# Kernel optimization log

Measured on AMD Instinct MI355X. Metric: run time of the kernel, lower is better.

Reference implementation:

```python
import jax, jax.numpy as jnp
import numpy as np

SEQ, B, V, E, H, L = 64, 64, 32000, 512, 512, 2


def setup_inputs() -> dict:
    key = jax.random.key(0)
    ks = jax.random.split(key, 12)
    k = float(np.sqrt(1.0 / H))
    u = lambda kk, shape, a, b: jax.random.uniform(kk, shape, jnp.float32, a, b)
    return {
        "inputs": jax.random.randint(ks[0], (SEQ, B), 0, V),          # [T, B] token ids
        "hidden": jnp.zeros((L, B, H), jnp.float32),                   # initial hidden
        "emb": u(ks[1], (V, E), -0.1, 0.1),                            # embedding table
        "Wr_w": u(ks[2], (L, H, E + H), -k, k),                        # reset gate [L,H,2H]
        "Wr_b": u(ks[3], (L, H), -k, k),
        "Wz_w": u(ks[4], (L, H, E + H), -k, k),                        # update gate
        "Wz_b": u(ks[5], (L, H), -k, k),
        "Wh_w": u(ks[6], (L, H, E + H), -k, k),                        # candidate
        "Wh_b": u(ks[7], (L, H), -k, k),
        "out_w": u(ks[8], (V, H), -0.1, 0.1),                          # output projection
        "out_b": jnp.zeros((V,), jnp.float32),
    }


def reference(inputs, hidden, emb, Wr_w, Wr_b, Wz_w, Wz_b, Wh_w, Wh_b, out_w, out_b):
    # GRU recurrence over time via lax.scan (dropout disabled: dp_keep_prob=1.0)
    def step(h, tok):
        x = emb[tok]  # [B, E]
        new_h = []
        for i in range(L):  # fixed small layer loop
            hi = h[i]  # [B, H]
            cat = jnp.concatenate([x, hi], axis=1)  # [B, E+H]
            r = jax.nn.sigmoid(cat @ Wr_w[i].T + Wr_b[i])
            z = jax.nn.sigmoid(cat @ Wz_w[i].T + Wz_b[i])
            h_hat = jnp.tanh(jnp.concatenate([x, r * hi], axis=1) @ Wh_w[i].T + Wh_b[i])
            x = (1.0 - z) * hi + z * h_hat  # next layer input / new hidden
            new_h.append(x)
        logits_t = x @ out_w.T + out_b  # [B, V]
        return jnp.stack(new_h), logits_t

    hidden_final, logits = jax.lax.scan(step, hidden, inputs)
    return logits, hidden_final  # [T,B,V], [L,B,H]
```

## Files before the change

kernel.cpp:

```cpp
#include <hip/hip_runtime.h>

constexpr int NT = 64;
constexpr int NB = 64;
constexpr int NV = 32000;
constexpr int NE = 512;
constexpr int NH = 512;
constexpr int NPAIR = 16 * 250;

constexpr size_t SZ_OW  = (size_t)NV * NE;
constexpr size_t SZ_XE  = (size_t)NT * NB * NE;
constexpr size_t SZ_H   = (size_t)NB * NH;
constexpr size_t LOGITS = (size_t)NT * NB * NV;

typedef float f32x4 __attribute__((ext_vector_type(4)));
typedef int   i32x4 __attribute__((ext_vector_type(4)));
typedef short bf16x8 __attribute__((ext_vector_type(8)));
typedef short s16x4 __attribute__((ext_vector_type(4)));
typedef _Float16 f16x8 __attribute__((ext_vector_type(8)));

__device__ __forceinline__ unsigned short f2bf(float x) {
  unsigned u = __float_as_uint(x);
  u += 0x7FFFu + ((u >> 16) & 1u);
  return (unsigned short)(u >> 16);
}
__device__ __forceinline__ float bf2f(unsigned short s) {
  return __uint_as_float(((unsigned)s) << 16);
}
__device__ __forceinline__ void split2(float v, short* hi, short* lo) {
  unsigned short h = f2bf(v);
  *hi = (short)h;
  *lo = (short)f2bf(v - bf2f(h));
}
__device__ __forceinline__ f32x4 mma_bf16(bf16x8 a, bf16x8 b, f32x4 c) {
  return __builtin_amdgcn_mfma_f32_16x16x32_bf16(a, b, c, 0, 0, 0);
}
__device__ __forceinline__ f32x4 mma_f16(f16x8 a, f16x8 b, f32x4 c) {
  return __builtin_amdgcn_mfma_f32_16x16x32_f16(a, b, c, 0, 0, 0);
}
__device__ __forceinline__ float fast_sigmoid(float x) {
  return __builtin_amdgcn_rcpf(1.0f + __expf(-x));
}
__device__ __forceinline__ float fast_tanh(float x) {
  return 1.0f - 2.0f * __builtin_amdgcn_rcpf(1.0f + __expf(2.0f * x));
}

__device__ __forceinline__ void st_sc32u(unsigned* p, unsigned v) {
  asm volatile("global_store_dword %0, %1, off sc0 sc1" :: "v"(p), "v"(v) : "memory");
}
__device__ __forceinline__ void st_sc128(void* p, i32x4 v) {
  asm volatile("global_store_dwordx4 %0, %1, off sc0 sc1" :: "v"(p), "v"(v) : "memory");
}
__device__ __forceinline__ void st_nt(float* p, float v) {
  asm volatile("global_store_dword %0, %1, off nt" :: "v"(p), "v"(v) : "memory");
}
__device__ __forceinline__ unsigned ld_sc32u(const unsigned* p) {
  unsigned v;
  asm volatile("global_load_dword %0, %1, off sc0 sc1\n\ts_waitcnt vmcnt(0)"
               : "=v"(v) : "v"(p) : "memory");
  return v;
}

__device__ __forceinline__ void wait1(const unsigned* flags, int slot, unsigned thr) {
  while (ld_sc32u(&flags[(size_t)slot * 32]) < thr) {}
}
__device__ __forceinline__ void wave_poll4(const unsigned* flags, int slotBase, int cgBase,
                                           int rh, unsigned thr, int lane) {
  const unsigned* fp = &flags[(size_t)(slotBase + (cgBase + (lane & 3)) * 2 + rh) * 32];
  while (!__all((int)(ld_sc32u(fp) >= thr))) {}
}
__device__ __forceinline__ void wave_poll8(const unsigned* flags, int slotBase, int cgBase,
                                           int rh, unsigned thr, int lane) {
  const unsigned* fp = &flags[(size_t)(slotBase + (cgBase + (lane & 7)) * 2 + rh) * 32];
  while (!__all((int)(ld_sc32u(fp) >= thr))) {}
}

__device__ __forceinline__ void publish(unsigned* flags, int slot, unsigned val) {
  asm volatile("s_waitcnt vmcnt(0)" ::: "memory");
  __syncthreads();
  if (threadIdx.x == 0) st_sc32u(&flags[(size_t)slot * 32], val);
}

__global__ void k_prep(
    const float* __restrict__ outw, const int* __restrict__ toks,
    const float* __restrict__ emb, const float* __restrict__ hid,
    _Float16* OWf, short* XeHi, short* XeLo,
    short* X1Hi, short* X1Lo, short* h0Hi, short* h0Lo) {
  const size_t stride = (size_t)gridDim.x * blockDim.x;
  const size_t N1 = SZ_OW, N2 = N1 + SZ_XE, N3 = N2 + SZ_H, N4 = N3 + SZ_H;
  for (size_t x = (size_t)blockIdx.x * blockDim.x + threadIdx.x; x < N4; x += stride) {
    if (x < N1) {
      OWf[x] = (_Float16)outw[x];
    } else if (x < N2) {
      size_t p = x - N1;
      size_t r = p >> 9, c = p & 511u;
      int tok = toks[r];
      float v = emb[(size_t)tok * 512 + c];
      short hi, lo; split2(v, &hi, &lo);
      XeHi[p] = hi; XeLo[p] = lo;
    } else if (x < N3) {
      size_t p = x - N2;
      short hi, lo; split2(hid[p], &hi, &lo);
      h0Hi[p] = hi; h0Lo[p] = lo;
    } else {
      size_t p = x - N3;
      short hi, lo; split2(hid[SZ_H + p], &hi, &lo);
      X1Hi[p] = hi; X1Lo[p] = lo;
    }
  }
}

__device__ __forceinline__ void mmaP32(
    const short* __restrict__ aH, const short* __restrict__ aL, int base,
    const short* lsHi_, const short* lsLo_,
    f32x4 (&accH)[2], f32x4 (&accL)[2], int wave, int l15, int lq) {
  const int kq = wave >> 1, rhalf = wave & 1;
  const int r0 = rhalf * 16 + l15;
#pragma unroll
  for (int i = 0; i < 4; ++i) {
    const int ko = kq * 128 + i * 32 + lq * 8;
    const int kg = base + ko;
    const int e0 = (l15 * 1024 + kg) ^ ((l15 & 7) << 3);
    const int e1 = ((16 + l15) * 1024 + kg) ^ ((l15 & 7) << 3);
    bf16x8 bh0 = *(const bf16x8*)&lsHi_[e0];
    bf16x8 bl0 = *(const bf16x8*)&lsLo_[e0];
    bf16x8 bh1 = *(const bf16x8*)&lsHi_[e1];
    bf16x8 bl1 = *(const bf16x8*)&lsLo_[e1];
    bf16x8 ah = *(const bf16x8*)&aH[r0 * 512 + ko];
    bf16x8 al = *(const bf16x8*)&aL[r0 * 512 + ko];
    accH[0] = mma_bf16(ah, bh0, accH[0]);
    accH[1] = mma_bf16(ah, bh1, accH[1]);
    accL[0] = mma_bf16(al, bh0, accL[0]);
    accL[1] = mma_bf16(al, bh1, accL[1]);
    accL[0] = mma_bf16(ah, bl0, accL[0]);
    accL[1] = mma_bf16(ah, bl1, accL[1]);
  }
}
__device__ __forceinline__ void reduce4(float* lsRed_, f32x4 (&accH)[2], f32x4 (&accL)[2],
                                        f32x4 (&acc)[2], int wave, int l15, int lq) {
  const int kq = wave >> 1, rhalf = wave & 1;
  acc[0] = accH[0] + accL[0];
  acc[1] = accH[1] + accL[1];
  const int pos = l15 * 16 + lq * 4;
  if (kq) {
    *(f32x4*)&lsRed_[(((kq - 1) * 2 + rhalf) * 2 + 0) * 256 + pos] = acc[0];
    *(f32x4*)&lsRed_[(((kq - 1) * 2 + rhalf) * 2 + 1) * 256 + pos] = acc[1];
  }
  __syncthreads();
  if (!kq) {
#pragma unroll
    for (int s = 0; s < 3; ++s) {
      acc[0] += *(const f32x4*)&lsRed_[((s * 2 + rhalf) * 2 + 0) * 256 + pos];
      acc[1] += *(const f32x4*)&lsRed_[((s * 2 + rhalf) * 2 + 1) * 256 + pos];
    }
  }
  __syncthreads();
}

__device__ __forceinline__ void mmaD(
    const short* __restrict__ pAH, const short* __restrict__ pAL,
    int kloc0, int kkGlob0, const short* lsHi_, const short* lsLo_,
    f32x4 (&accH)[2], f32x4 (&accL)[2], int l15, int lq, int rhalf, int rowbase) {
  const int r0 = rowbase + rhalf * 16 + l15;
#pragma unroll 4
  for (int i = 0; i < 8; ++i) {
    const int kk = kkGlob0 + i * 32 + lq * 8;
    const int ka = kloc0 + i * 32 + lq * 8;
    const int e0 = (l15 * 1024 + kk) ^ ((l15 & 7) << 3);
    const int e1 = ((16 + l15) * 1024 + kk) ^ ((l15 & 7) << 3);
    bf16x8 bh0 = *(const bf16x8*)&lsHi_[e0];
    bf16x8 bl0 = *(const bf16x8*)&lsLo_[e0];
    bf16x8 bh1 = *(const bf16x8*)&lsHi_[e1];
    bf16x8 bl1 = *(const bf16x8*)&lsLo_[e1];
    bf16x8 ah = *(const bf16x8*)&pAH[r0 * 512 + ka];
    bf16x8 al = *(const bf16x8*)&pAL[r0 * 512 + ka];
    accH[0] = mma_bf16(ah, bh0, accH[0]);
    accH[1] = mma_bf16(ah, bh1, accH[1]);
    accL[0] = mma_bf16(al, bh0, accL[0]);
    accL[1] = mma_bf16(al, bh1, accL[1]);
    accL[0] = mma_bf16(ah, bl0, accL[0]);
    accL[1] = mma_bf16(ah, bl1, accL[1]);
  }
}
__device__ __forceinline__ void reduceD(float* lsRed_, f32x4 (&accH)[2], f32x4 (&accL)[2],
                                        f32x4 (&acc)[2], int wave, int l15, int lq) {
  acc[0] = accH[0] + accL[0];
  acc[1] = accH[1] + accL[1];
  const int pos = l15 * 16 + lq * 4;
  if (wave >= 2) {
    *(f32x4*)&lsRed_[((wave - 2) * 2 + 0) * 256 + pos] = acc[0];
    *(f32x4*)&lsRed_[((wave - 2) * 2 + 1) * 256 + pos] = acc[1];
  }
  __syncthreads();
  if (wave < 2) {
#pragma unroll
    for (int s = 0; s < 3; ++s) {
      const int slot = (wave & 1) + 2 * s;
      acc[0] += *(const f32x4*)&lsRed_[(slot * 2 + 0) * 256 + pos];
      acc[1] += *(const f32x4*)&lsRed_[(slot * 2 + 1) * 256 + pos];
    }
  }
  __syncthreads();
}

__device__ __forceinline__ void stage_weights(
    short* lsHi, short* lsLo, const float* srcBase0, const float* srcBase1,
    int jc, int tid) {
  for (int i = tid; i < 8192; i += 512) {
    const int j = i >> 8;
    const int k4 = (i & 255) << 2;
    const int g = jc + j;
    const float* src = (srcBase1 && g >= 512)
        ? (srcBase1 + (size_t)(g - 512) * 1024 + k4)
        : (srcBase0 + (size_t)g * 1024 + k4);
    f32x4 v = *(const f32x4*)src;
    s16x4 h4, l4;
#pragma unroll
    for (int q = 0; q < 4; ++q) { short hi, lo; split2(v[q], &hi, &lo); h4[q] = hi; l4[q] = lo; }
    const int els = (j * 1024 + k4) ^ ((j & 7) << 3);
    *(s16x4*)&lsHi[els] = h4;
    *(s16x4*)&lsLo[els] = l4;
  }
}

__device__ void gemm_loop(char* pool, int tid,
                          const _Float16* Af, const _Float16* Bw,
                          const float* bias, float* C,
                          unsigned* flags, unsigned* tcnt) {
  _Float16* lsA0 = (_Float16*)pool;
  _Float16* lsA1 = lsA0 + 128 * 64;
  _Float16* lsB  = lsA1 + 128 * 64;
  volatile int* bc = (volatile int*)(pool + 49152);
  const int wave = tid >> 6, lane = tid & 63, l15 = lane & 15, lq = lane >> 4;
  const int wr = (wave >> 2) * 64, wc = (wave & 3) * 32;
  unsigned lastR = 0;
  __syncthreads();
  for (;;) {
    if (tid == 0)
      *bc = (int)__hip_atomic_fetch_add(tcnt, 1u, __ATOMIC_RELAXED,
                                        __HIP_MEMORY_SCOPE_AGENT);
    __syncthreads();
    const int pr = *bc;
    __syncthreads();
    if (pr >= NPAIR) break;
    const int p = pr / 250, bn = pr - p * 250;
    const unsigned Rneed = 4u * (unsigned)p + 4u;
    if (lastR < Rneed) {
      if (tid < 32) {
        const unsigned* fp = &flags[(size_t)(160 + tid) * 32];
        while (ld_sc32u(fp) < Rneed) __builtin_amdgcn_s_sleep(8);
      }
      lastR = Rneed;
    }
    __syncthreads();
    f32x4 acc0[4][2] = {}, acc1[4][2] = {};
    const size_t arow0 = (size_t)p * 256;
    const size_t brow0 = (size_t)bn * 128;
    for (int kb = 0; kb < 512; kb += 64) {
#pragma unroll
      for (int i = 0; i < 2; ++i) {
        int c = tid + i * 512;
        int row = c >> 3, kc = (c & 7) * 8;
        int el = (row * 64 + kc) ^ ((row & 7) << 3);
        *(f16x8*)&lsA0[el] = *(const f16x8*)(Af + (arow0 + row) * 512 + kb + kc);
        *(f16x8*)&lsA1[el] = *(const f16x8*)(Af + (arow0 + 128 + row) * 512 + kb + kc);
        *(f16x8*)&lsB[el]  = *(const f16x8*)(Bw + (brow0 + row) * 512 + kb + kc);
      }
      __syncthreads();
#pragma unroll
      for (int k0 = 0; k0 < 64; k0 += 32) {
        const int kk = k0 + lq * 8;
        f16x8 af0[4], af1[4], bfr[2];
#pragma unroll
        for (int i = 0; i < 4; ++i) {
          int ra = wr + i * 16 + l15;
          int el = (ra * 64 + kk) ^ ((ra & 7) << 3);
          af0[i] = *(const f16x8*)&lsA0[el];
          af1[i] = *(const f16x8*)&lsA1[el];
        }
#pragma unroll
        for (int jt = 0; jt < 2; ++jt) {
          int rb = wc + jt * 16 + l15;
          bfr[jt] = *(const f16x8*)&lsB[(rb * 64 + kk) ^ ((rb & 7) << 3)];
        }
#pragma unroll
        for (int i = 0; i < 4; ++i)
#pragma unroll
          for (int jt = 0; jt < 2; ++jt) {
            acc0[i][jt] = mma_f16(af0[i], bfr[jt], acc0[i][jt]);
            acc1[i][jt] = mma_f16(af1[i], bfr[jt], acc1[i][jt]);
          }
      }
      __syncthreads();
    }
    const float b0v = bias[brow0 + wc + l15];
    const float b1v = bias[brow0 + wc + 16 + l15];
#pragma unroll
    for (int i = 0; i < 4; ++i) {
#pragma unroll
      for (int r = 0; r < 4; ++r) {
        const size_t row = arow0 + wr + i * 16 + lq * 4 + r;
        float* pa = C + row * (size_t)NV + brow0 + wc + l15;
        st_nt(pa, acc0[i][0][r] + b0v);
        st_nt(pa + 16, acc0[i][1][r] + b1v);
        float* pb = pa + (size_t)128 * NV;
        st_nt(pb, acc1[i][0][r] + b0v);
        st_nt(pb + 16, acc1[i][1][r] + b1v);
      }
    }
  }
}

__launch_bounds__(512, 1)
__global__ void k_main(
    const float* __restrict__ Wr, const float* __restrict__ Wz, const float* __restrict__ Wh,
    const float* __restrict__ Wrb, const float* __restrict__ Wzb, const float* __restrict__ Whb,
    const short* __restrict__ XeHi, const short* __restrict__ XeLo,
    short* X1Hi, short* X1Lo, _Float16* X1f16,
    short* h0Hi, short* h0Lo,
    short* rh0Hi, short* rh0Lo, short* rh1Hi, short* rh1Lo,
    float* z0, float* z1, float* hidOut,
    const _Float16* OWf, const float* outb, float* out,
    unsigned* flags, unsigned* tcnt) {
  __shared__ __align__(16) char pool[153600];
  short* lsHi = (short*)pool;
  short* lsLo = lsHi + 32 * 1024;
  float* lsRed = (float*)(pool + 131072);
  short* sH    = (short*)(pool + 131072);
  short* sL    = sH + 1024;
  float* sZA   = (float*)(pool + 131072);
  short* stH   = (short*)(pool + 143360);
  short* stL   = stH + 1024;
  float* sZ    = (float*)(pool + 147456);
  _Float16* sX = (_Float16*)(pool + 151552);

  const int wg = blockIdx.x;
  const int tid = threadIdx.x;
  const int wave = tid >> 6, lane = tid & 63, l15 = lane & 15, lq = lane >> 4;

  if (wg < 64) {
    const int cg = wg >> 1, rh = wg & 1, jc = cg * 32, rowbase = rh * 32;
    const bool isR = (jc < 512);
    stage_weights(lsHi, lsLo, Wr, Wz, jc, tid);
    float biasL0, biasL1;
    {
      const int j0 = jc + l15, j1 = j0 + 16;
      biasL0 = (j0 < 512) ? Wrb[j0] : Wzb[j0 - 512];
      biasL1 = (j1 < 512) ? Wrb[j1] : Wzb[j1 - 512];
    }
    __syncthreads();
    for (int t = 0; t < NT; ++t) {
      f32x4 accH[2] = {}, accL[2] = {};
      mmaP32(XeHi + (size_t)t * SZ_H + rowbase * 512,
             XeLo + (size_t)t * SZ_H + rowbase * 512, 0,
             lsHi, lsLo, accH, accL, wave, l15, lq);
      const short* hH = h0Hi + (size_t)t * SZ_H + rowbase * 512;
      const short* hL = h0Lo + (size_t)t * SZ_H + rowbase * 512;
      i32x4 pre;
      const int pbuf = tid >> 7, pq = tid & 127, prow = pq >> 2, pc = pq & 3;
      if (isR && tid < 256) {
        wait1(flags, 128 + ((jc >> 5) * 2 + rh), (unsigned)t);
        pre = *(const i32x4*)((pbuf ? hL : hH) + prow * 512 + jc + pc * 8);
      }
      wave_poll4(flags, 128, 4 * (wave >> 1), rh, (unsigned)t, lane);
      mmaP32(hH, hL, 512, lsHi, lsLo, accH, accL, wave, l15, lq);
      if (isR && tid < 256)
        *(i32x4*)&(pbuf ? stL : stH)[prow * 32 + pc * 8] = pre;
      f32x4 acc[2];
      reduce4(lsRed, accH, accL, acc, wave, l15, lq);
      if (wave < 2) {
#pragma unroll
        for (int ct = 0; ct < 2; ++ct) {
          const int jj = ct * 16 + l15;
          const float bv = ct ? biasL1 : biasL0;
#pragma unroll
          for (int r = 0; r < 4; ++r) {
            const int lb = wave * 16 + lq * 4 + r;
            const float s = fast_sigmoid(acc[ct][r] + bv);
            if (isR) {
              const float hv = bf2f((unsigned short)stH[lb * 32 + jj]) +
                               bf2f((unsigned short)stL[lb * 32 + jj]);
              short hi, lo; split2(s * hv, &hi, &lo);
              sH[lb * 32 + jj] = hi; sL[lb * 32 + jj] = lo;
            } else {
              sZA[lb * 32 + jj] = s;
            }
          }
        }
      }
      __syncthreads();
      if (isR) {
        if (tid < 256) {
          i32x4 v = *(const i32x4*)&(pbuf ? sL : sH)[prow * 32 + pc * 8];
          st_sc128((pbuf ? rh0Lo : rh0Hi) + (size_t)t * SZ_H +
                   (size_t)(rowbase + prow) * 512 + jc + pc * 8, v);
        }
      } else {
        if (tid < 256) {
          const int row = tid >> 3, c = tid & 7;
          i32x4 v = *(const i32x4*)&sZA[row * 32 + c * 4];
          st_sc128(z0 + (size_t)t * SZ_H + (size_t)(rowbase + row) * 512 +
                   (jc - 512) + c * 4, v);
        }
      }
      publish(flags, wg, (unsigned)(t + 1));
    }
  } else if (wg < 128) {
    const int idx = wg - 64, cg = idx >> 1, rh = idx & 1, jc = cg * 32, rowbase = rh * 32;
    const bool isR = (jc < 512);
    stage_weights(lsHi, lsLo, Wr + (size_t)512 * 1024, Wz + (size_t)512 * 1024, jc, tid);
    float biasL0, biasL1;
    {
      const int j0 = jc + l15, j1 = j0 + 16;
      biasL0 = (j0 < 512) ? Wrb[512 + j0] : Wzb[512 + j0 - 512];
      biasL1 = (j1 < 512) ? Wrb[512 + j1] : Wzb[512 + j1 - 512];
    }
    __syncthreads();
    for (int t = 0; t < NT; ++t) {
      const short* xH = h0Hi + (size_t)(t + 1) * SZ_H;
      const short* xL = h0Lo + (size_t)(t + 1) * SZ_H;
      const short* hH = X1Hi + (size_t)t * SZ_H;
      const short* hL = X1Lo + (size_t)t * SZ_H;
      i32x4 pre;
      const int pbuf = tid >> 7, pq = tid & 127, prow = pq >> 2, pc = pq & 3;
      if (isR && tid < 256) {
        wait1(flags, 160 + ((jc >> 5) * 2 + rh), (unsigned)t);
        pre = *(const i32x4*)((pbuf ? hL : hH) +
                              (size_t)(rowbase + prow) * 512 + jc + pc * 8);
      }
      f32x4 accH[2] = {}, accL[2] = {};
      {
        const int khalf = wave >> 1, rhalf = wave & 1;
        if (khalf < 2) wave_poll8(flags, 128, (khalf & 1) * 8, rh, (unsigned)(t + 1), lane);
        else           wave_poll8(flags, 160, (khalf & 1) * 8, rh, (unsigned)t, lane);
        const short* pAH = (khalf < 2) ? xH : hH;
        const short* pAL = (khalf < 2) ? xL : hL;
        mmaD(pAH, pAL, (khalf & 1) * 256, khalf * 256, lsHi, lsLo,
             accH, accL, l15, lq, rhalf, rowbase);
      }
      if (isR && tid < 256)
        *(i32x4*)&(pbuf ? stL : stH)[prow * 32 + pc * 8] = pre;
      f32x4 acc[2];
      reduceD(lsRed, accH, accL, acc, wave, l15, lq);
      if (wave < 2) {
#pragma unroll
        for (int ct = 0; ct < 2; ++ct) {
          const int jj = ct * 16 + l15;
          const float bv = ct ? biasL1 : biasL0;
#pragma unroll
          for (int r = 0; r < 4; ++r) {
            const int lb = wave * 16 + lq * 4 + r;
            const float s = fast_sigmoid(acc[ct][r] + bv);
            if (isR) {
              const float hv = bf2f((unsigned short)stH[lb * 32 + jj]) +
                               bf2f((unsigned short)stL[lb * 32 + jj]);
              short hi, lo; split2(s * hv, &hi, &lo);
              sH[lb * 32 + jj] = hi; sL[lb * 32 + jj] = lo;
            } else {
              sZA[lb * 32 + jj] = s;
            }
          }
        }
      }
      __syncthreads();
      if (isR) {
        if (tid < 256) {
          i32x4 v = *(const i32x4*)&(pbuf ? sL : sH)[prow * 32 + pc * 8];
          st_sc128((pbuf ? rh1Lo : rh1Hi) + (size_t)t * SZ_H +
                   (size_t)(rowbase + prow) * 512 + jc + pc * 8, v);
        }
      } else {
        if (tid < 256) {
          const int row = tid >> 3, c = tid & 7;
          i32x4 v = *(const i32x4*)&sZA[row * 32 + c * 4];
          st_sc128(z1 + (size_t)t * SZ_H + (size_t)(rowbase + row) * 512 +
                   (jc - 512) + c * 4, v);
        }
      }
      publish(flags, wg, (unsigned)(t + 1));
    }
  } else if (wg < 192) {
    const bool isL1 = (wg >= 160);
    const int idx = isL1 ? (wg - 160) : (wg - 128);
    const int cg = idx >> 1, rh = idx & 1, jc = cg * 32, rowbase = rh * 32;
    const int layer = isL1 ? 1 : 0;
    stage_weights(lsHi, lsLo, Wh + (size_t)layer * 512 * 1024, nullptr, jc, tid);
    const float biasL0 = Whb[layer * 512 + jc + l15];
    const float biasL1 = Whb[layer * 512 + jc + 16 + l15];
    __syncthreads();
    short* myHi = isL1 ? X1Hi : h0Hi;
    short* myLo = isL1 ? X1Lo : h0Lo;
    const short* rhHi_ = isL1 ? rh1Hi : rh0Hi;
    const short* rhLo_ = isL1 ? rh1Lo : rh0Lo;
    const float* zArr = isL1 ? z1 : z0;
    const int fbase = isL1 ? 64 : 0;
    for (int t = 0; t < NT; ++t) {
      const int pbuf = tid >> 7, pq = tid & 127, prow = pq >> 2, pc = pq & 3;
      if (tid < 256) {
        const short* src = (pbuf ? myLo : myHi) + (size_t)t * SZ_H +
                           (size_t)(rowbase + prow) * 512 + jc + pc * 8;
        *(i32x4*)&(pbuf ? stL : stH)[prow * 32 + pc * 8] = *(const i32x4*)src;
      }
      f32x4 accH[2] = {}, accL[2] = {};
      if (isL1) {
        wave_poll4(flags, 128, 4 * (wave >> 1), rh, (unsigned)(t + 1), lane);
        mmaP32(h0Hi + (size_t)(t + 1) * SZ_H + rowbase * 512,
               h0Lo + (size_t)(t + 1) * SZ_H + rowbase * 512, 0,
               lsHi, lsLo, accH, accL, wave, l15, lq);
      } else {
        mmaP32(XeHi + (size_t)t * SZ_H + rowbase * 512,
               XeLo + (size_t)t * SZ_H + rowbase * 512, 0,
               lsHi, lsLo, accH, accL, wave, l15, lq);
      }
      f32x4 zv;
      const int zrow = tid >> 3, zc = tid & 7;
      if (tid < 256) {
        wait1(flags, fbase + ((16 + (jc >> 5)) * 2 + rh), (unsigned)(t + 1));
        zv = *(const f32x4*)(zArr + (size_t)t * SZ_H +
                             (size_t)(rowbase + zrow) * 512 + jc + zc * 4);
      }
      wave_poll4(flags, fbase, 4 * (wave >> 1), rh, (unsigned)(t + 1), lane);
      mmaP32(rhHi_ + (size_t)t * SZ_H + rowbase * 512,
             rhLo_ + (size_t)t * SZ_H + rowbase * 512, 512,
             lsHi, lsLo, accH, accL, wave, l15, lq);
      if (tid < 256)
        *(f32x4*)&sZ[zrow * 32 + zc * 4] = zv;
      f32x4 acc[2];
      reduce4(lsRed, accH, accL, acc, wave, l15, lq);
      if (wave < 2) {
#pragma unroll
        for (int ct = 0; ct < 2; ++ct) {
          const int jj = ct * 16 + l15, j = jc + jj;
          const float bv = ct ? biasL1 : biasL0;
#pragma unroll
          for (int r = 0; r < 4; ++r) {
            const int lb = wave * 16 + lq * 4 + r;
            const float hh = fast_tanh(acc[ct][r] + bv);
            const float z = sZ[lb * 32 + jj];
            const float ho = bf2f((unsigned short)stH[lb * 32 + jj]) +
                             bf2f((unsigned short)stL[lb * 32 + jj]);
            const float hn = (1.0f - z) * ho + z * hh;
            short hi, lo; split2(hn, &hi, &lo);
            sH[lb * 32 + jj] = hi; sL[lb * 32 + jj] = lo;
            if (isL1) sX[lb * 32 + jj] = (_Float16)hn;
            if (t == NT - 1)
              hidOut[(size_t)layer * SZ_H + (size_t)(rowbase + lb) * 512 + j] = hn;
          }
        }
      }
      __syncthreads();
      if (tid < 256) {
        i32x4 v = *(const i32x4*)&(pbuf ? sL : sH)[prow * 32 + pc * 8];
        st_sc128((pbuf ? myLo : myHi) + (size_t)(t + 1) * SZ_H +
                 (size_t)(rowbase + prow) * 512 + jc + pc * 8, v);
      } else if (isL1 && tid < 384) {
        const int q = tid - 256, row = q >> 2, c = q & 3;
        i32x4 v = *(const i32x4*)&sX[row * 32 + c * 8];
        st_sc128(X1f16 + (size_t)t * SZ_H + (size_t)(rowbase + row) * 512 + jc + c * 8, v);
      }
      publish(flags, wg, (unsigned)(t + 1));
    }
  }
  gemm_loop(pool, tid, X1f16, OWf, outb, out, flags, tcnt);
}

extern "C" void kernel_launch(void* const* d_in, const int* in_sizes, int n_in,
                              void* d_out, int out_size, void* d_ws, size_t ws_size,
                              hipStream_t stream) {
  (void)in_sizes; (void)n_in; (void)out_size; (void)ws_size;
  const int*   toks = (const int*)d_in[0];
  const float* hid  = (const float*)d_in[1];
  const float* emb  = (const float*)d_in[2];
  const float* Wr   = (const float*)d_in[3];
  const float* Wrb  = (const float*)d_in[4];
  const float* Wz   = (const float*)d_in[5];
  const float* Wzb  = (const float*)d_in[6];
  const float* Wh   = (const float*)d_in[7];
  const float* Whb  = (const float*)d_in[8];
  const float* outw = (const float*)d_in[9];
  const float* outb = (const float*)d_in[10];
  float* out = (float*)d_out;

  char* base = (char*)d_ws;
  size_t off = 0;
  auto carve = [&](size_t bytes) -> char* {
    char* r = base + off;
    off = (off + bytes + 255) & ~(size_t)255;
    return r;
  };
  _Float16* OWf   = (_Float16*)carve(SZ_OW * 2);
  short*    XeHi  = (short*)carve(SZ_XE * 2);
  short*    XeLo  = (short*)carve(SZ_XE * 2);
  short*    X1Hi  = (short*)carve((size_t)(NT + 1) * SZ_H * 2);
  short*    X1Lo  = (short*)carve((size_t)(NT + 1) * SZ_H * 2);
  _Float16* X1f16 = (_Float16*)carve((size_t)NT * SZ_H * 2);
  short*    h0Hi  = (short*)carve((size_t)(NT + 1) * SZ_H * 2);
  short*    h0Lo  = (short*)carve((size_t)(NT + 1) * SZ_H * 2);
  short*    rh0Hi = (short*)carve((size_t)NT * SZ_H * 2);
  short*    rh0Lo = (short*)carve((size_t)NT * SZ_H * 2);
  short*    rh1Hi = (short*)carve((size_t)NT * SZ_H * 2);
  short*    rh1Lo = (short*)carve((size_t)NT * SZ_H * 2);
  float*    z0    = (float*)carve((size_t)NT * SZ_H * 4);
  float*    z1    = (float*)carve((size_t)NT * SZ_H * 4);
  unsigned* flags = (unsigned*)carve(32768);
  unsigned* tcnt  = (unsigned*)carve(256);

  hipMemsetAsync(flags, 0, 32768, stream);
  hipMemsetAsync(tcnt, 0, 256, stream);

  k_prep<<<2048, 256, 0, stream>>>(outw, toks, emb, hid,
                                   OWf, XeHi, XeLo, X1Hi, X1Lo, h0Hi, h0Lo);

  k_main<<<256, 512, 0, stream>>>(
      Wr, Wz, Wh, Wrb, Wzb, Whb, XeHi, XeLo,
      X1Hi, X1Lo, X1f16, h0Hi, h0Lo,
      rh0Hi, rh0Lo, rh1Hi, rh1Lo, z0, z1,
      out + LOGITS, OWf, outb, out, flags, tcnt);
}
```

Baseline: 698.4 us.

## Widen output GEMM tiles to 256x256 and merge flag polls into one wave poll

The output-projection GEMM tile grows from 256x128 to 256x256, giving 2000 work quads instead of 4000 pairs. Each A tile loaded into LDS now feeds twice as many MFMAs, and per-tile scheduling and flag-wait overhead is halved. The cost is a doubling of accumulator registers and a larger LDS footprint, which may cause spills. Separately, the single-thread wait1 spin and the wave-wide poll in the recurrent stages are folded into one wave poll, with one lane assigned to the extra flag, to cut serialized polling latency.

Result: no change. 703.2 us (+0.7%).

```diff
diff --git a/kernel.cpp b/kernel.cpp
--- a/kernel.cpp
+++ b/kernel.cpp
@@ -5,7 +5,7 @@
 constexpr int NV = 32000;
 constexpr int NE = 512;
 constexpr int NH = 512;
-constexpr int NPAIR = 16 * 250;
+constexpr int NQUAD = 16 * 125;
 
 constexpr size_t SZ_OW  = (size_t)NV * NE;
 constexpr size_t SZ_XE  = (size_t)NT * NB * NE;
@@ -60,18 +60,13 @@
   return v;
 }
 
-__device__ __forceinline__ void wait1(const unsigned* flags, int slot, unsigned thr) {
-  while (ld_sc32u(&flags[(size_t)slot * 32]) < thr) {}
+__device__ __forceinline__ void wave_poll(const unsigned* fp, unsigned thr) {
+  while (!__all((int)(ld_sc32u(fp) >= thr))) {}
 }
 __device__ __forceinline__ void wave_poll4(const unsigned* flags, int slotBase, int cgBase,
                                            int rh, unsigned thr, int lane) {
   const unsigned* fp = &flags[(size_t)(slotBase + (cgBase + (lane & 3)) * 2 + rh) * 32];
-  while (!__all((int)(ld_sc32u(fp) >= thr))) {}
-}
-__device__ __forceinline__ void wave_poll8(const unsigned* flags, int slotBase, int cgBase,
-                                           int rh, unsigned thr, int lane) {
-  const unsigned* fp = &flags[(size_t)(slotBase + (cgBase + (lane & 7)) * 2 + rh) * 32];
-  while (!__all((int)(ld_sc32u(fp) >= thr))) {}
+  wave_poll(fp, thr);
 }
 
 __device__ __forceinline__ void publish(unsigned* flags, int slot, unsigned val) {
@@ -227,9 +222,10 @@
                           const float* bias, float* C,
                           unsigned* flags, unsigned* tcnt) {
   _Float16* lsA0 = (_Float16*)pool;
-  _Float16* lsA1 = lsA0 + 128 * 64;
-  _Float16* lsB  = lsA1 + 128 * 64;
-  volatile int* bc = (volatile int*)(pool + 49152);
+  _Float16* lsA1 = lsA0 + 8192;
+  _Float16* lsB0 = lsA1 + 8192;
+  _Float16* lsB1 = lsB0 + 8192;
+  volatile int* bc = (volatile int*)(pool + 65536);
   const int wave = tid >> 6, lane = tid & 63, l15 = lane & 15, lq = lane >> 4;
   const int wr = (wave >> 2) * 64, wc = (wave & 3) * 32;
   unsigned lastR = 0;
@@ -241,8 +237,8 @@
     __syncthreads();
     const int pr = *bc;
     __syncthreads();
-    if (pr >= NPAIR) break;
-    const int p = pr / 250, bn = pr - p * 250;
+    if (pr >= NQUAD) break;
+    const int p = pr / 125, bq = pr - p * 125;
     const unsigned Rneed = 4u * (unsigned)p + 4u;
     if (lastR < Rneed) {
       if (tid < 32) {
@@ -252,9 +248,9 @@
       lastR = Rneed;
     }
     __syncthreads();
-    f32x4 acc0[4][2] = {}, acc1[4][2] = {};
+    f32x4 a00[4][2] = {}, a01[4][2] = {}, a10[4][2] = {}, a11[4][2] = {};
     const size_t arow0 = (size_t)p * 256;
-    const size_t brow0 = (size_t)bn * 128;
+    const size_t brow0 = (size_t)bq * 256;
     for (int kb = 0; kb < 512; kb += 64) {
 #pragma unroll
       for (int i = 0; i < 2; ++i) {
@@ -263,13 +259,14 @@
         int el = (row * 64 + kc) ^ ((row & 7) << 3);
         *(f16x8*)&lsA0[el] = *(const f16x8*)(Af + (arow0 + row) * 512 + kb + kc);
         *(f16x8*)&lsA1[el] = *(const f16x8*)(Af + (arow0 + 128 + row) * 512 + kb + kc);
-        *(f16x8*)&lsB[el]  = *(const f16x8*)(Bw + (brow0 + row) * 512 + kb + kc);
+        *(f16x8*)&lsB0[el] = *(const f16x8*)(Bw + (brow0 + row) * 512 + kb + kc);
+        *(f16x8*)&lsB1[el] = *(const f16x8*)(Bw + (brow0 + 128 + row) * 512 + kb + kc);
       }
       __syncthreads();
 #pragma unroll
       for (int k0 = 0; k0 < 64; k0 += 32) {
         const int kk = k0 + lq * 8;
-        f16x8 af0[4], af1[4], bfr[2];
+        f16x8 af0[4], af1[4], b0[2], b1[2];
 #pragma unroll
         for (int i = 0; i < 4; ++i) {
           int ra = wr + i * 16 + l15;
@@ -280,31 +277,41 @@
 #pragma unroll
         for (int jt = 0; jt < 2; ++jt) {
           int rb = wc + jt * 16 + l15;
-          bfr[jt] = *(const f16x8*)&lsB[(rb * 64 + kk) ^ ((rb & 7) << 3)];
+          int el = (rb * 64 + kk) ^ ((rb & 7) << 3);
+          b0[jt] = *(const f16x8*)&lsB0[el];
+          b1[jt] = *(const f16x8*)&lsB1[el];
         }
 #pragma unroll
         for (int i = 0; i < 4; ++i)
 #pragma unroll
           for (int jt = 0; jt < 2; ++jt) {
-            acc0[i][jt] = mma_f16(af0[i], bfr[jt], acc0[i][jt]);
-            acc1[i][jt] = mma_f16(af1[i], bfr[jt], acc1[i][jt]);
+            a00[i][jt] = mma_f16(af0[i], b0[jt], a00[i][jt]);
+            a01[i][jt] = mma_f16(af0[i], b1[jt], a01[i][jt]);
+            a10[i][jt] = mma_f16(af1[i], b0[jt], a10[i][jt]);
+            a11[i][jt] = mma_f16(af1[i], b1[jt], a11[i][jt]);
           }
       }
       __syncthreads();
     }
-    const float b0v = bias[brow0 + wc + l15];
-    const float b1v = bias[brow0 + wc + 16 + l15];
+    const float c00 = bias[brow0 + wc + l15];
+    const float c01 = bias[brow0 + wc + 16 + l15];
+    const float c10 = bias[brow0 + 128 + wc + l15];
+    const float c11 = bias[brow0 + 128 + wc + 16 + l15];
 #pragma unroll
     for (int i = 0; i < 4; ++i) {
 #pragma unroll
       for (int r = 0; r < 4; ++r) {
         const size_t row = arow0 + wr + i * 16 + lq * 4 + r;
         float* pa = C + row * (size_t)NV + brow0 + wc + l15;
-        st_nt(pa, acc0[i][0][r] + b0v);
-        st_nt(pa + 16, acc0[i][1][r] + b1v);
+        st_nt(pa, a00[i][0][r] + c00);
+        st_nt(pa + 16, a00[i][1][r] + c01);
+        st_nt(pa + 128, a01[i][0][r] + c10);
+        st_nt(pa + 144, a01[i][1][r] + c11);
         float* pb = pa + (size_t)128 * NV;
-        st_nt(pb, acc1[i][0][r] + b0v);
-        st_nt(pb + 16, acc1[i][1][r] + b1v);
+        st_nt(pb, a10[i][0][r] + c00);
+        st_nt(pb + 16, a10[i][1][r] + c01);
+        st_nt(pb + 128, a11[i][0][r] + c10);
+        st_nt(pb + 144, a11[i][1][r] + c11);
       }
     }
   }
@@ -355,13 +362,17 @@
              lsHi, lsLo, accH, accL, wave, l15, lq);
       const short* hH = h0Hi + (size_t)t * SZ_H + rowbase * 512;
       const short* hL = h0Lo + (size_t)t * SZ_H + rowbase * 512;
+      {
+        const int idx = lane & 7;
+        int cgp = 4 * (wave >> 1) + (idx & 3);
+        if (idx == 4 && isR) cgp = (jc >> 5);
+        const unsigned* fp = &flags[(size_t)(128 + cgp * 2 + rh) * 32];
+        wave_poll(fp, (unsigned)t);
+      }
       i32x4 pre;
       const int pbuf = tid >> 7, pq = tid & 127, prow = pq >> 2, pc = pq & 3;
-      if (isR && tid < 256) {
-        wait1(flags, 128 + ((jc >> 5) * 2 + rh), (unsigned)t);
+      if (isR && tid < 256)
         pre = *(const i32x4*)((pbuf ? hL : hH) + prow * 512 + jc + pc * 8);
-      }
-      wave_poll4(flags, 128, 4 * (wave >> 1), rh, (unsigned)t, lane);
       mmaP32(hH, hL, 512, lsHi, lsLo, accH, accL, wave, l15, lq);
       if (isR && tid < 256)
         *(i32x4*)&(pbuf ? stL : stH)[prow * 32 + pc * 8] = pre;
@@ -405,7 +416,7 @@
       publish(flags, wg, (unsigned)(t + 1));
     }
   } else if (wg < 128) {
-    const int idx = wg - 64, cg = idx >> 1, rh = idx & 1, jc = cg * 32, rowbase = rh * 32;
+    const int idx0 = wg - 64, cg = idx0 >> 1, rh = idx0 & 1, jc = cg * 32, rowbase = (idx0 & 1) * 32;
     const bool isR = (jc < 512);
     stage_weights(lsHi, lsLo, Wr + (size_t)512 * 1024, Wz + (size_t)512 * 1024, jc, tid);
     float biasL0, biasL1;
@@ -420,18 +431,28 @@
       const short* xL = h0Lo + (size_t)(t + 1) * SZ_H;
       const short* hH = X1Hi + (size_t)t * SZ_H;
       const short* hL = X1Lo + (size_t)t * SZ_H;
+      const int khalf = wave >> 1, rhalf = wave & 1;
+      {
+        const int idx = lane & 15;
+        const unsigned* fp; unsigned thr;
+        if (idx == 8 && isR) {
+          fp = &flags[(size_t)(160 + (jc >> 5) * 2 + rh) * 32]; thr = (unsigned)t;
+        } else if (khalf < 2) {
+          const int cgp = (khalf & 1) * 8 + (idx & 7);
+          fp = &flags[(size_t)(128 + cgp * 2 + rh) * 32]; thr = (unsigned)(t + 1);
+        } else {
+          const int cgp = (khalf & 1) * 8 + (idx & 7);
+          fp = &flags[(size_t)(160 + cgp * 2 + rh) * 32]; thr = (unsigned)t;
+        }
+        wave_poll(fp, thr);
+      }
       i32x4 pre;
       const int pbuf = tid >> 7, pq = tid & 127, prow = pq >> 2, pc = pq & 3;
-      if (isR && tid < 256) {
-        wait1(flags, 160 + ((jc >> 5) * 2 + rh), (unsigned)t);
+      if (isR && tid < 256)
         pre = *(const i32x4*)((pbuf ? hL : hH) +
                               (size_t)(rowbase + prow) * 512 + jc + pc * 8);
-      }
       f32x4 accH[2] = {}, accL[2] = {};
       {
-        const int khalf = wave >> 1, rhalf = wave & 1;
-        if (khalf < 2) wave_poll8(flags, 128, (khalf & 1) * 8, rh, (unsigned)(t + 1), lane);
-        else           wave_poll8(flags, 160, (khalf & 1) * 8, rh, (unsigned)t, lane);
         const short* pAH = (khalf < 2) ? xH : hH;
         const short* pAL = (khalf < 2) ? xL : hL;
         mmaD(pAH, pAL, (khalf & 1) * 256, khalf * 256, lsHi, lsLo,
@@ -480,8 +501,8 @@
     }
   } else if (wg < 192) {
     const bool isL1 = (wg >= 160);
-    const int idx = isL1 ? (wg - 160) : (wg - 128);
-    const int cg = idx >> 1, rh = idx & 1, jc = cg * 32, rowbase = rh * 32;
+    const int idx0 = isL1 ? (wg - 160) : (wg - 128);
+    const int cg = idx0 >> 1, rh = idx0 & 1, jc = cg * 32, rowbase = (idx0 & 1) * 32;
     const int layer = isL1 ? 1 : 0;
     stage_weights(lsHi, lsLo, Wh + (size_t)layer * 512 * 1024, nullptr, jc, tid);
     const float biasL0 = Whb[layer * 512 + jc + l15];
@@ -511,14 +532,18 @@
                XeLo + (size_t)t * SZ_H + rowbase * 512, 0,
                lsHi, lsLo, accH, accL, wave, l15, lq);
       }
+      {
+        const int idx = lane & 7;
+        int cgp = 4 * (wave >> 1) + (idx & 3);
+        if (idx == 4) cgp = 16 + (jc >> 5);
+        const unsigned* fp = &flags[(size_t)(fbase + cgp * 2 + rh) * 32];
+        wave_poll(fp, (unsigned)(t + 1));
+      }
       f32x4 zv;
       const int zrow = tid >> 3, zc = tid & 7;
-      if (tid < 256) {
-        wait1(flags, fbase + ((16 + (jc >> 5)) * 2 + rh), (unsigned)(t + 1));
+      if (tid < 256)
         zv = *(const f32x4*)(zArr + (size_t)t * SZ_H +
                              (size_t)(rowbase + zrow) * 512 + jc + zc * 4);
-      }
-      wave_poll4(flags, fbase, 4 * (wave >> 1), rh, (unsigned)(t + 1), lane);
       mmaP32(rhHi_ + (size_t)t * SZ_H + rowbase * 512,
              rhLo_ + (size_t)t * SZ_H + rowbase * 512, 512,
              lsHi, lsLo, accH, accL, wave, l15, lq);
```
